# Optimization experiments

Measured on AMD Instinct MI355X. Metric: run time of the kernel, lower is better.

## Reference

```python
import jax, jax.numpy as jnp
import numpy as np

N = 1_000_000
H = 128
G = 4096


def setup_inputs() -> dict:
    key = jax.random.key(0)
    k1, k2, k3, k4 = jax.random.split(key, 4)
    x = jax.random.normal(k1, (N, H), dtype=jnp.float32)
    batch = jnp.sort(jax.random.randint(k2, (N,), 0, G, dtype=jnp.int64))
    w1 = jax.random.normal(k3, (H, H), dtype=jnp.float32) * 0.05
    b1 = jnp.zeros((H,), dtype=jnp.float32)
    w2 = jax.random.normal(k4, (H, 1), dtype=jnp.float32) * 0.05
    b2 = jnp.zeros((1,), dtype=jnp.float32)
    return {"x": x, "batch": batch, "w1": w1, "b1": b1, "w2": w2, "b2": b2, "num_graphs": G}


def reference(x, batch, w1, b1, w2, b2, num_graphs):
    # attention MLP: Linear -> Tanh -> Linear(->1)
    s = (jnp.tanh(x @ w1 + b1) @ w2 + b2)[:, 0]  # [N]
    # segmented (per-graph) stable softmax
    smax = jax.ops.segment_max(s, batch, num_segments=num_graphs)  # [G]
    smax = jnp.where(jnp.isfinite(smax), smax, 0.0)  # guard empty graphs
    e = jnp.exp(s - smax[batch])  # [N]
    denom = jax.ops.segment_sum(e, batch, num_segments=num_graphs)  # [G]
    w = e / jnp.where(denom > 0, denom, 1.0)[batch]  # [N]
    # weighted sum pooling per graph -> [G, H]
    pooled = jax.ops.segment_sum(x * w[:, None], batch, num_segments=num_graphs)
    return pooled
```

## Files before the change

### kernel.cpp

```cpp
#include <hip/hip_runtime.h>
#include <math.h>

#define H 128

typedef float f32x4 __attribute__((ext_vector_type(4)));
typedef __bf16 bf16x8 __attribute__((ext_vector_type(8)));

__device__ __forceinline__ float fast_tanh(float v) {
    float e = __expf(2.0f * v);
    float r = __builtin_amdgcn_rcpf(e + 1.0f);
    return fmaf(-2.0f, r, 1.0f);
}

__global__ __launch_bounds__(512, 2) void k_fused(
    const float* __restrict__ x, const int* __restrict__ batch,
    const float* __restrict__ w1, const float* __restrict__ b1,
    const float* __restrict__ w2, float* __restrict__ out,
    float* __restrict__ denom, int n, int ntiles)
{
    __shared__ __bf16 wsm[2 * H * H];

    const int tid = threadIdx.x;

    for (int idx = tid; idx < H * H; idx += 512) {
        int k = idx >> 7, nn = idx & 127;
        float v = w1[idx];
        __bf16 h = (__bf16)v;
        __bf16 l = (__bf16)(v - (float)h);
        int c = (k >> 3) ^ (nn & 15);
        int pos = nn * H + c * 8 + (k & 7);
        wsm[pos] = h;
        wsm[H * H + pos] = l;
    }

    const int wv = tid >> 6;
    const int lane = tid & 63;
    const int p = lane & 15;
    const int q = lane >> 4;

    const bool is64 = (batch[n - 1] == 0);

    __syncthreads();

    for (int tile = blockIdx.x; tile < ntiles; tile += (int)gridDim.x) {
        const long long base = (long long)tile * 128 + wv * 16;

        bf16x8 ah[4], al[4];
        const long long r0 = base + p;
        const bool ok = (r0 < (long long)n);
        {
            const float4* rp = (const float4*)(x + r0 * H);
            #pragma unroll
            for (int kc = 0; kc < 4; ++kc) {
                float4 u0 = {0.f, 0.f, 0.f, 0.f}, u1 = {0.f, 0.f, 0.f, 0.f};
                if (ok) { u0 = rp[kc * 8 + q * 2]; u1 = rp[kc * 8 + q * 2 + 1]; }
                float vals[8] = {u0.x, u0.y, u0.z, u0.w, u1.x, u1.y, u1.z, u1.w};
                #pragma unroll
                for (int j = 0; j < 8; ++j) {
                    __bf16 h = (__bf16)vals[j];
                    ah[kc][j] = h;
                    al[kc][j] = (__bf16)(vals[j] - (float)h);
                }
            }
        }

        float part[4] = {0.f, 0.f, 0.f, 0.f};

        #pragma unroll
        for (int nt = 0; nt < 8; ++nt) {
            const int nn = nt * 16 + p;
            f32x4 acc = {0.f, 0.f, 0.f, 0.f};
            #pragma unroll
            for (int kc = 0; kc < 4; ++kc) {
                const int c = (kc * 4 + q) ^ p;
                const __bf16* bb = &wsm[nn * H + c * 8];
                bf16x8 bh = *(const bf16x8*)bb;
                bf16x8 bl = *(const bf16x8*)(bb + H * H);
                acc = __builtin_amdgcn_mfma_f32_16x16x32_bf16(ah[kc], bh, acc, 0, 0, 0);
                acc = __builtin_amdgcn_mfma_f32_16x16x32_bf16(al[kc], bh, acc, 0, 0, 0);
                acc = __builtin_amdgcn_mfma_f32_16x16x32_bf16(ah[kc], bl, acc, 0, 0, 0);
            }
            const float b1v = b1[nn];
            const float w2v = w2[nn];
            #pragma unroll
            for (int rg = 0; rg < 4; ++rg)
                part[rg] = fmaf(fast_tanh(acc[rg] + b1v), w2v, part[rg]);
        }

        #pragma unroll
        for (int off = 1; off < 16; off <<= 1) {
            #pragma unroll
            for (int rg = 0; rg < 4; ++rg)
                part[rg] += __shfl_xor(part[rg], off);
        }

        float e;
        {
            const int srcl = (p >> 2) * 16;
            float a0 = __shfl(part[0], srcl);
            float a1 = __shfl(part[1], srcl);
            float a2 = __shfl(part[2], srcl);
            float a3 = __shfl(part[3], srcl);
            int rs = p & 3;
            float sv = (rs == 0) ? a0 : (rs == 1) ? a1 : (rs == 2) ? a2 : a3;
            e = ok ? __expf(sv) : 0.0f;
        }

        int ga = ok ? (is64 ? batch[(size_t)r0 * 2] : batch[r0]) : 0x7FFFFFFF;

        while (true) {
            int gm = ga;
            #pragma unroll
            for (int off = 1; off < 16; off <<= 1)
                gm = min(gm, __shfl_xor(gm, off));
            if (gm == 0x7FFFFFFF) break;

            float ea = (ga == gm) ? e : 0.0f;

            float dsum = ea;
            #pragma unroll
            for (int off = 1; off < 16; off <<= 1)
                dsum += __shfl_xor(dsum, off);
            if (lane == 0) atomicAdd(&denom[gm], dsum);

            #pragma unroll
            for (int kc = 0; kc < 4; ++kc) {
                float t[8];
                #pragma unroll
                for (int j = 0; j < 8; ++j)
                    t[j] = ea * ((float)ah[kc][j] + (float)al[kc][j]);
                #pragma unroll
                for (int off = 1; off < 16; off <<= 1) {
                    #pragma unroll
                    for (int j = 0; j < 8; ++j)
                        t[j] += __shfl_xor(t[j], off);
                }
                if (p == 0) {
                    float* ob = out + (size_t)gm * H + kc * 32 + q * 8;
                    #pragma unroll
                    for (int j = 0; j < 8; ++j)
                        atomicAdd(&ob[j], t[j]);
                }
            }

            if (ga == gm) ga = 0x7FFFFFFF;
        }
    }
}

__global__ void k_zero(float* __restrict__ out, float* __restrict__ denom,
                       int nf, int g_count)
{
    int i = blockIdx.x * blockDim.x + threadIdx.x;
    if (i < nf) out[i] = 0.0f;
    else if (i < nf + g_count) denom[i - nf] = 0.0f;
}

__global__ void k_norm(float* __restrict__ out, const float* __restrict__ denom,
                       int total4)
{
    int i = blockIdx.x * blockDim.x + threadIdx.x;
    if (i >= total4) return;
    int g = i >> 5;
    float d = denom[g];
    float inv = (d > 0.0f) ? (1.0f / d) : 1.0f;
    float4 v = ((float4*)out)[i];
    v.x *= inv; v.y *= inv; v.z *= inv; v.w *= inv;
    ((float4*)out)[i] = v;
}

extern "C" void kernel_launch(void* const* d_in, const int* in_sizes, int n_in,
                              void* d_out, int out_size, void* d_ws, size_t ws_size,
                              hipStream_t stream)
{
    const float* x     = (const float*)d_in[0];
    const int*   batch = (const int*)d_in[1];
    const float* w1    = (const float*)d_in[2];
    const float* b1    = (const float*)d_in[3];
    const float* w2    = (const float*)d_in[4];
    const int n = in_sizes[0] / H;
    const int G = out_size / H;
    float* out = (float*)d_out;

    float* denom = (float*)d_ws;

    const int nf = G * H;
    const int tiles = (n + 127) / 128;
    k_zero<<<(nf + G + 255) / 256, 256, 0, stream>>>(out, denom, nf, G);
    k_fused<<<1024, 512, 0, stream>>>(x, batch, w1, b1, w2, out, denom, n, tiles);
    k_norm<<<(G * 32 + 255) / 256, 256, 0, stream>>>(out, denom, G * 32);
}
```

Measured before the change: 1.278 ms.

## Accumulate per-graph pooling in shared-memory slots before flushing to global

Each block now handles 256-row tiles in two passes and accumulates weighted row sums and denominators into a small shared-memory slot array indexed relative to the tile's first graph. It falls back to global atomics only when a graph lies beyond the slots. At tile end it flushes slots to global memory, using plain stores for graphs wholly inside the tile and atomics for boundary graphs. This targets the high volume of global float atomics on the output, at the cost of extra block barriers, a zeroing pass per tile, and halving the number of tiles per grid sweep.

```diff
diff --git a/kernel.cpp b/kernel.cpp
--- a/kernel.cpp
+++ b/kernel.cpp
@@ -2,6 +2,7 @@
 #include <math.h>
 
 #define H 128
+#define SLOTS 8
 
 typedef float f32x4 __attribute__((ext_vector_type(4)));
 typedef __bf16 bf16x8 __attribute__((ext_vector_type(8)));
@@ -10,6 +11,11 @@
     float e = __expf(2.0f * v);
     float r = __builtin_amdgcn_rcpf(e + 1.0f);
     return fmaf(-2.0f, r, 1.0f);
+}
+
+__device__ __forceinline__ int bload(const int* __restrict__ batch, bool is64,
+                                     long long i) {
+    return is64 ? batch[(size_t)i * 2] : batch[i];
 }
 
 __global__ __launch_bounds__(512, 2) void k_fused(
@@ -19,6 +25,8 @@
     float* __restrict__ denom, int n, int ntiles)
 {
     __shared__ __bf16 wsm[2 * H * H];
+    __shared__ float accS[SLOTS * H];
+    __shared__ float accD[SLOTS];
 
     const int tid = threadIdx.x;
 
@@ -43,108 +51,153 @@
     __syncthreads();
 
     for (int tile = blockIdx.x; tile < ntiles; tile += (int)gridDim.x) {
-        const long long base = (long long)tile * 128 + wv * 16;
-
-        bf16x8 ah[4], al[4];
-        const long long r0 = base + p;
-        const bool ok = (r0 < (long long)n);
-        {
-            const float4* rp = (const float4*)(x + r0 * H);
+        const long long tbase = (long long)tile * 256;
+
+        for (int i = tid; i < SLOTS * H; i += 512) accS[i] = 0.0f;
+        if (tid < SLOTS) accD[tid] = 0.0f;
+        const int gfirst = bload(batch, is64, tbase);
+        __syncthreads();
+
+        for (int pass = 0; pass < 2; ++pass) {
+            const long long base = tbase + pass * 128 + wv * 16;
+            const long long r0 = base + p;
+            const bool ok = (r0 < (long long)n);
+
+            bf16x8 ah[4], al[4];
+            {
+                const float4* rp = (const float4*)(x + r0 * H);
+                #pragma unroll
+                for (int kc = 0; kc < 4; ++kc) {
+                    float4 u0 = {0.f, 0.f, 0.f, 0.f}, u1 = {0.f, 0.f, 0.f, 0.f};
+                    if (ok) { u0 = rp[kc * 8 + q * 2]; u1 = rp[kc * 8 + q * 2 + 1]; }
+                    float vals[8] = {u0.x, u0.y, u0.z, u0.w, u1.x, u1.y, u1.z, u1.w};
+                    #pragma unroll
+                    for (int j = 0; j < 8; ++j) {
+                        __bf16 h = (__bf16)vals[j];
+                        ah[kc][j] = h;
+                        al[kc][j] = (__bf16)(vals[j] - (float)h);
+                    }
+                }
+            }
+
+            float part[4] = {0.f, 0.f, 0.f, 0.f};
             #pragma unroll
-            for (int kc = 0; kc < 4; ++kc) {
-                float4 u0 = {0.f, 0.f, 0.f, 0.f}, u1 = {0.f, 0.f, 0.f, 0.f};
-                if (ok) { u0 = rp[kc * 8 + q * 2]; u1 = rp[kc * 8 + q * 2 + 1]; }
-                float vals[8] = {u0.x, u0.y, u0.z, u0.w, u1.x, u1.y, u1.z, u1.w};
-                #pragma unroll
-                for (int j = 0; j < 8; ++j) {
-                    __bf16 h = (__bf16)vals[j];
-                    ah[kc][j] = h;
-                    al[kc][j] = (__bf16)(vals[j] - (float)h);
-                }
-            }
-        }
-
-        float part[4] = {0.f, 0.f, 0.f, 0.f};
-
-        #pragma unroll
-        for (int nt = 0; nt < 8; ++nt) {
-            const int nn = nt * 16 + p;
-            f32x4 acc = {0.f, 0.f, 0.f, 0.f};
+            for (int nt = 0; nt < 8; ++nt) {
+                const int nn = nt * 16 + p;
+                f32x4 acc = {0.f, 0.f, 0.f, 0.f};
+                #pragma unroll
+                for (int kc = 0; kc < 4; ++kc) {
+                    const int c = (kc * 4 + q) ^ p;
+                    const __bf16* bb = &wsm[nn * H + c * 8];
+                    bf16x8 bh = *(const bf16x8*)bb;
+                    bf16x8 bl = *(const bf16x8*)(bb + H * H);
+                    acc = __builtin_amdgcn_mfma_f32_16x16x32_bf16(ah[kc], bh, acc, 0, 0, 0);
+                    acc = __builtin_amdgcn_mfma_f32_16x16x32_bf16(al[kc], bh, acc, 0, 0, 0);
+                    acc = __builtin_amdgcn_mfma_f32_16x16x32_bf16(ah[kc], bl, acc, 0, 0, 0);
+                }
+                const float b1v = b1[nn];
+                const float w2v = w2[nn];
+                #pragma unroll
+                for (int rg = 0; rg < 4; ++rg)
+                    part[rg] = fmaf(fast_tanh(acc[rg] + b1v), w2v, part[rg]);
+            }
+
             #pragma unroll
-            for (int kc = 0; kc < 4; ++kc) {
-                const int c = (kc * 4 + q) ^ p;
-                const __bf16* bb = &wsm[nn * H + c * 8];
-                bf16x8 bh = *(const bf16x8*)bb;
-                bf16x8 bl = *(const bf16x8*)(bb + H * H);
-                acc = __builtin_amdgcn_mfma_f32_16x16x32_bf16(ah[kc], bh, acc, 0, 0, 0);
-                acc = __builtin_amdgcn_mfma_f32_16x16x32_bf16(al[kc], bh, acc, 0, 0, 0);
-                acc = __builtin_amdgcn_mfma_f32_16x16x32_bf16(ah[kc], bl, acc, 0, 0, 0);
-            }
-            const float b1v = b1[nn];
-            const float w2v = w2[nn];
-            #pragma unroll
-            for (int rg = 0; rg < 4; ++rg)
-                part[rg] = fmaf(fast_tanh(acc[rg] + b1v), w2v, part[rg]);
-        }
-
-        #pragma unroll
-        for (int off = 1; off < 16; off <<= 1) {
-            #pragma unroll
-            for (int rg = 0; rg < 4; ++rg)
-                part[rg] += __shfl_xor(part[rg], off);
-        }
-
-        float e;
-        {
-            const int srcl = (p >> 2) * 16;
-            float a0 = __shfl(part[0], srcl);
-            float a1 = __shfl(part[1], srcl);
-            float a2 = __shfl(part[2], srcl);
-            float a3 = __shfl(part[3], srcl);
-            int rs = p & 3;
-            float sv = (rs == 0) ? a0 : (rs == 1) ? a1 : (rs == 2) ? a2 : a3;
-            e = ok ? __expf(sv) : 0.0f;
-        }
-
-        int ga = ok ? (is64 ? batch[(size_t)r0 * 2] : batch[r0]) : 0x7FFFFFFF;
-
-        while (true) {
-            int gm = ga;
-            #pragma unroll
-            for (int off = 1; off < 16; off <<= 1)
-                gm = min(gm, __shfl_xor(gm, off));
-            if (gm == 0x7FFFFFFF) break;
-
-            float ea = (ga == gm) ? e : 0.0f;
-
-            float dsum = ea;
-            #pragma unroll
-            for (int off = 1; off < 16; off <<= 1)
-                dsum += __shfl_xor(dsum, off);
-            if (lane == 0) atomicAdd(&denom[gm], dsum);
-
-            #pragma unroll
-            for (int kc = 0; kc < 4; ++kc) {
-                float t[8];
-                #pragma unroll
-                for (int j = 0; j < 8; ++j)
-                    t[j] = ea * ((float)ah[kc][j] + (float)al[kc][j]);
-                #pragma unroll
-                for (int off = 1; off < 16; off <<= 1) {
+            for (int off = 1; off < 16; off <<= 1) {
+                #pragma unroll
+                for (int rg = 0; rg < 4; ++rg)
+                    part[rg] += __shfl_xor(part[rg], off);
+            }
+
+            float e;
+            {
+                const int srcl = (p >> 2) * 16;
+                float a0 = __shfl(part[0], srcl);
+                float a1 = __shfl(part[1], srcl);
+                float a2 = __shfl(part[2], srcl);
+                float a3 = __shfl(part[3], srcl);
+                int rs = p & 3;
+                float sv = (rs == 0) ? a0 : (rs == 1) ? a1 : (rs == 2) ? a2 : a3;
+                e = ok ? __expf(sv) : 0.0f;
+            }
+
+            int ga = ok ? bload(batch, is64, r0) : 0x7FFFFFFF;
+
+            while (true) {
+                int gm = ga;
+                #pragma unroll
+                for (int off = 1; off < 16; off <<= 1)
+                    gm = min(gm, __shfl_xor(gm, off));
+                if (gm == 0x7FFFFFFF) break;
+
+                float ea = (ga == gm) ? e : 0.0f;
+                float dsum = ea;
+                #pragma unroll
+                for (int off = 1; off < 16; off <<= 1)
+                    dsum += __shfl_xor(dsum, off);
+
+                const int slot = gm - gfirst;
+
+                #pragma unroll
+                for (int kc = 0; kc < 4; ++kc) {
+                    float t[8];
                     #pragma unroll
                     for (int j = 0; j < 8; ++j)
-                        t[j] += __shfl_xor(t[j], off);
-                }
-                if (p == 0) {
-                    float* ob = out + (size_t)gm * H + kc * 32 + q * 8;
+                        t[j] = ea * ((float)ah[kc][j] + (float)al[kc][j]);
                     #pragma unroll
-                    for (int j = 0; j < 8; ++j)
-                        atomicAdd(&ob[j], t[j]);
-                }
-            }
-
-            if (ga == gm) ga = 0x7FFFFFFF;
+                    for (int off = 1; off < 16; off <<= 1) {
+                        #pragma unroll
+                        for (int j = 0; j < 8; ++j)
+                            t[j] += __shfl_xor(t[j], off);
+                    }
+                    if (p == 0) {
+                        if (slot < SLOTS) {
+                            float* ob = &accS[slot * H + kc * 32 + q * 8];
+                            #pragma unroll
+                            for (int j = 0; j < 8; ++j) atomicAdd(&ob[j], t[j]);
+                        } else {
+                            float* ob = out + (size_t)gm * H + kc * 32 + q * 8;
+                            #pragma unroll
+                            for (int j = 0; j < 8; ++j) atomicAdd(&ob[j], t[j]);
+                        }
+                    }
+                }
+                if (lane == 0) {
+                    if (slot < SLOTS) atomicAdd(&accD[slot], dsum);
+                    else atomicAdd(&denom[gm], dsum);
+                }
+
+                if (ga == gm) ga = 0x7FFFFFFF;
+            }
         }
+
+        __syncthreads();
+
+        {
+            const long long lastr =
+                (tbase + 255 < (long long)n) ? tbase + 255 : (long long)n - 1;
+            const int glast = bload(batch, is64, lastr);
+            for (int i = tid; i < SLOTS * H; i += 512) {
+                const int slot = i >> 7, c = i & 127;
+                const int g = gfirst + slot;
+                const float v = accS[i];
+                if (v != 0.0f) {
+                    if (g > gfirst && g < glast)
+                        out[(size_t)g * H + c] = v;
+                    else
+                        atomicAdd(&out[(size_t)g * H + c], v);
+                }
+            }
+            if (tid < SLOTS) {
+                const int g = gfirst + tid;
+                const float d = accD[tid];
+                if (d != 0.0f) {
+                    if (g > gfirst && g < glast) denom[g] = d;
+                    else atomicAdd(&denom[g], d);
+                }
+            }
+        }
+        __syncthreads();
     }
 }
 
@@ -185,7 +238,7 @@
     float* denom = (float*)d_ws;
 
     const int nf = G * H;
-    const int tiles = (n + 127) / 128;
+    const int tiles = (n + 255) / 256;
     k_zero<<<(nf + G + 255) / 256, 256, 0, stream>>>(out, denom, nf, G);
     k_fused<<<1024, 512, 0, stream>>>(x, batch, w1, b1, w2, out, denom, n, tiles);
     k_norm<<<(G * 32 + 255) / 256, 256, 0, stream>>>(out, denom, G * 32);
```

Result: slower. 1.440 ms (+12.6%).
